# Optimization experiments

Hardware: AMD Instinct MI355X
Metric: run time of the kernel (lower is better)

## Reference

```python
import jax, jax.numpy as jnp
import numpy as np

MARGIN = 70.0
THR = 125.0
PD_EPS = 1e-6  # torch F.pairwise_distance default eps


def _return_cam(features, weight_softmax, class_idx):
    # features: [bz, nc, h, w]; weight_softmax: [n_cls, nc]; class_idx: [bz]
    w_sel = weight_softmax[class_idx]                     # [bz, nc]
    cam = jnp.einsum('bc,bchw->bhw', w_sel, features)     # [bz, h, w]
    cam = cam - cam.min(axis=(1, 2), keepdims=True)
    cam = cam / cam.max(axis=(1, 2), keepdims=True) * 255.0
    return cam[:, None]                                   # [bz, 1, h, w]


def _pairwise_distance(x, y):
    # torch F.pairwise_distance: ||x - y + eps||_2 along last dim
    return jnp.sqrt(jnp.sum((x - y + PD_EPS) ** 2, axis=-1))


def setup_inputs() -> dict:
    key = jax.random.key(0)
    ks = jax.random.split(key, 6)
    bz, nc, h, w, n_cls = 64, 2048, 14, 14, 1000
    return {
        'pred': jax.random.normal(ks[0], (bz, n_cls), jnp.float32),
        'cla_truth': jax.random.randint(ks[1], (bz,), 0, n_cls, jnp.int32),
        'seg_truth': jax.random.uniform(ks[2], (bz, h, w), jnp.float32),
        'features_blobs': jax.random.normal(ks[3], (bz, nc, h, w), jnp.float32),
        'weight_softmax': jax.random.normal(ks[4], (n_cls, nc), jnp.float32),
        'idx': jax.random.randint(ks[5], (bz, 3), 0, n_cls, jnp.int32),
    }


def reference(pred, cla_truth, seg_truth, features_blobs, weight_softmax, idx):
    bz, nc, h, w = features_blobs.shape
    # cross entropy
    logp = jax.nn.log_softmax(pred, axis=-1)
    loss1 = -jnp.mean(logp[jnp.arange(bz), cla_truth])
    # CAMs for top-3 predicted classes
    cam0 = _return_cam(features_blobs, weight_softmax, idx[:, 0])  # [bz,1,h,w]
    cam1 = _return_cam(features_blobs, weight_softmax, idx[:, 1])
    cam2 = _return_cam(features_blobs, weight_softmax, idx[:, 2])
    # binarize cam0 (values in [0,255]); <=thr -> 0, >thr -> 1
    dst = jnp.where(cam0[:, 0] > THR, 1.0, 0.0)                     # [bz,h,w]
    # row-wise distance to seg truth, averaged over rows
    ed1 = jnp.mean(_pairwise_distance(dst, seg_truth), axis=1)      # [bz]
    # CAM-weighted features via broadcasted matmul (requires h == w)
    fea0 = jnp.matmul(cam0, features_blobs)                         # [bz,nc,h,w]
    fea1 = jnp.matmul(cam1, features_blobs)
    fea2 = jnp.matmul(cam2, features_blobs)
    d01 = _pairwise_distance(fea0.reshape(bz, -1), fea1.reshape(bz, -1)) / nc
    d02 = _pairwise_distance(fea0.reshape(bz, -1), fea2.reshape(bz, -1)) / nc
    loss_dis = jnp.mean(ed1 + jnp.clip(MARGIN - d01 - d02, 0.0, None)) + loss1
    return loss_dis
```

## Files before the change

kernel.cpp:

```cpp
#include <hip/hip_runtime.h>
#include <hip/hip_bf16.h>
#include <math.h>

#define BZ      64
#define NC      2048
#define HH      14
#define HW      196
#define NCLS    1000
#define SPLITS  8
#define CPB     (NC/SPLITS)
#define CHUNK   8
#define NCHUNK  (CPB/CHUNK)

#define CAM_OFF  0
#define G_OFF    (BZ*SPLITS*3*HW)
#define S_OFF    (G_OFF + BZ*SPLITS*HW)
#define TERM_OFF (S_OFF + BZ*SPLITS*HH)

__global__ __launch_bounds__(320) void k_stage1(
    const float* __restrict__ F, const float* __restrict__ W,
    const int* __restrict__ idx, float* __restrict__ ws)
{
  __shared__ __align__(16) float Fs[2][CHUNK*HW];
  __shared__ __align__(16) float wls[3][CPB];
  __shared__ __align__(16) float sred[HW];
  __shared__ __align__(16) float gred[224*4];

  const int t = threadIdx.x;
  const int s = blockIdx.x;
  const int b = blockIdx.y;
  const int cbase = s*CPB;

  const int i0 = idx[b*3+0], i1 = idx[b*3+1], i2 = idx[b*3+2];
  if (t < CPB){
    wls[0][t] = W[(size_t)i0*NC + cbase + t];
    wls[1][t] = W[(size_t)i1*NC + cbase + t];
    wls[2][t] = W[(size_t)i2*NC + cbase + t];
  }

  const float* Fb = F + ((size_t)b*NC + cbase)*HW;

  const bool isCam = (t < 49);
  const bool isG   = (t >= 64 && t < 288);
  int m0=0,m1=0,n0=0,n1=0, cg=0, tmKeep=0, tnKeep=0;
  if (isG){
    int g = t - 64;
    int tile = g % 28; cg = g / 28;
    int k = tile, tm = 0;
    while (k >= 7 - tm){ k -= 7 - tm; tm++; }
    int tn = tm + k;
    tmKeep = tm; tnKeep = tn;
    m0 = 2*tm; m1 = m0+1; n0 = 2*tn; n1 = n0+1;
  }
  (void)tmKeep; (void)tnKeep;

  float4 c0a = make_float4(0.f,0.f,0.f,0.f);
  float4 c1a = make_float4(0.f,0.f,0.f,0.f);
  float4 c2a = make_float4(0.f,0.f,0.f,0.f);
  float4 sA  = make_float4(0.f,0.f,0.f,0.f);
  float g00=0.f, g01=0.f, g10=0.f, g11=0.f;

  float4 pre0 = make_float4(0.f,0.f,0.f,0.f);
  float4 pre1 = make_float4(0.f,0.f,0.f,0.f);

  auto loadChunk = [&](int ch){
    if (t < 196){
      const float4* src = (const float4*)(Fb + (size_t)ch*CHUNK*HW);
      pre0 = src[2*t]; pre1 = src[2*t+1];
    }
  };
  auto storeChunk = [&](int bufi){
    if (t < 196){
      float4* dst = (float4*)(&Fs[bufi][0]);
      dst[2*t] = pre0; dst[2*t+1] = pre1;
    }
  };

  loadChunk(0);
  storeChunk(0);
  __syncthreads();

  for (int ch = 0; ch < NCHUNK; ++ch){
    const int bufi = ch & 1;
    if (ch+1 < NCHUNK) loadChunk(ch+1);
    const float* Fsb = &Fs[bufi][0];

    if (isCam){
      float w0a[CHUNK], w1a[CHUNK], w2a[CHUNK];
      *(float4*)&w0a[0] = *(const float4*)&wls[0][ch*CHUNK];
      *(float4*)&w0a[4] = *(const float4*)&wls[0][ch*CHUNK+4];
      *(float4*)&w1a[0] = *(const float4*)&wls[1][ch*CHUNK];
      *(float4*)&w1a[4] = *(const float4*)&wls[1][ch*CHUNK+4];
      *(float4*)&w2a[0] = *(const float4*)&wls[2][ch*CHUNK];
      *(float4*)&w2a[4] = *(const float4*)&wls[2][ch*CHUNK+4];
      #pragma unroll
      for (int c=0;c<CHUNK;c++){
        float4 v = *(const float4*)(Fsb + c*HW + 4*t);
        c0a.x += w0a[c]*v.x; c0a.y += w0a[c]*v.y; c0a.z += w0a[c]*v.z; c0a.w += w0a[c]*v.w;
        c1a.x += w1a[c]*v.x; c1a.y += w1a[c]*v.y; c1a.z += w1a[c]*v.z; c1a.w += w1a[c]*v.w;
        c2a.x += w2a[c]*v.x; c2a.y += w2a[c]*v.y; c2a.z += w2a[c]*v.z; c2a.w += w2a[c]*v.w;
        sA.x += v.x; sA.y += v.y; sA.z += v.z; sA.w += v.w;
      }
    }
    if (isG){
      const float* Mb = Fsb + cg*HW;
      const float2* r0 = (const float2*)(Mb + m0*HH);
      const float2* r1 = (const float2*)(Mb + m1*HH);
      const float2* q0 = (const float2*)(Mb + n0*HH);
      const float2* q1 = (const float2*)(Mb + n1*HH);
      #pragma unroll
      for (int jj=0;jj<7;jj++){
        float2 a0=r0[jj], a1=r1[jj], b0=q0[jj], b1=q1[jj];
        g00 += a0.x*b0.x + a0.y*b0.y;
        g01 += a0.x*b1.x + a0.y*b1.y;
        g10 += a1.x*b0.x + a1.y*b0.y;
        g11 += a1.x*b1.x + a1.y*b1.y;
      }
    }
    if (ch+1 < NCHUNK) storeChunk((ch+1)&1);
    __syncthreads();
  }

  const size_t pslot = (size_t)(b*SPLITS + s);
  if (isCam){
    float* base = ws + CAM_OFF + pslot*3*HW;
    *(float4*)(base          + 4*t) = c0a;
    *(float4*)(base + HW     + 4*t) = c1a;
    *(float4*)(base + 2*HW   + 4*t) = c2a;
    *(float4*)(sred + 4*t) = sA;
  }
  if (isG){
    int g = t - 64;
    float* gr = &gred[g*4];
    gr[0]=g00; gr[1]=g01; gr[2]=g10; gr[3]=g11;
  }
  __syncthreads();

  if (t < HH){
    float acc=0.f;
    #pragma unroll
    for (int j=0;j<HH;j++) acc += sred[t*HH+j];
    ws[S_OFF + pslot*HH + t] = acc;
  }
  if (t < 112){
    int tile = t >> 2, q = t & 3;
    int k = tile, tm2 = 0;
    while (k >= 7 - tm2){ k -= 7 - tm2; tm2++; }
    int tn2 = tm2 + k;
    float acc=0.f;
    #pragma unroll
    for (int c=0;c<8;c++) acc += gred[(c*28+tile)*4 + q];
    int a = q>>1, bb = q&1;
    int mm = 2*tm2 + a, nn = 2*tn2 + bb;
    float* gb = ws + G_OFF + pslot*HW;
    gb[mm*HH+nn] = acc;
    if (tn2 > tm2) gb[nn*HH+mm] = acc;
  }
}

template<int MODE>
__device__ __forceinline__ float bred(float v, float* red){
  #pragma unroll
  for (int o=32;o>0;o>>=1){
    float u = __shfl_down(v, o, 64);
    if (MODE==0) v += u; else if (MODE==1) v = fminf(v,u); else v = fmaxf(v,u);
  }
  __syncthreads();
  if ((threadIdx.x & 63)==0) red[threadIdx.x>>6] = v;
  __syncthreads();
  float r = red[0];
  #pragma unroll
  for (int w=1;w<4;w++){
    float u = red[w];
    if (MODE==0) r += u; else if (MODE==1) r = fminf(r,u); else r = fmaxf(r,u);
  }
  return r;
}

__global__ __launch_bounds__(256) void k_stage2(
    const float* __restrict__ pred, const int* __restrict__ cla,
    const float* __restrict__ seg, float* __restrict__ ws)
{
  const int t = threadIdx.x, b = blockIdx.x;
  __shared__ float cam[3][HW], Gm[HW], Sv[HH];
  __shared__ float D1[HW], D2[HW], EE[HW];
  __shared__ float rowv[HH], dc1[HH], dc2[HH];
  __shared__ float red[4];
  __shared__ float scal[6];

  if (t < HW){
    for (int k=0;k<3;k++){
      float a=0.f;
      for (int s=0;s<SPLITS;s++)
        a += ws[CAM_OFF + ((size_t)(b*SPLITS+s)*3 + k)*HW + t];
      cam[k][t]=a;
    }
    float g=0.f;
    for (int s=0;s<SPLITS;s++) g += ws[G_OFF + (size_t)(b*SPLITS+s)*HW + t];
    Gm[t]=g;
  }
  if (t < HH){
    float a=0.f;
    for (int s=0;s<SPLITS;s++) a += ws[S_OFF + (size_t)(b*SPLITS+s)*HH + t];
    Sv[t]=a;
  }
  __syncthreads();

  for (int k=0;k<3;k++){
    float v = (t<HW)? cam[k][t] : 3.0e38f;
    float mn = bred<1>(v, red);
    v = (t<HW)? cam[k][t] : -3.0e38f;
    float mx = bred<2>(v, red);
    if (t==0){ scal[2*k]=mn; scal[2*k+1]=mx; }
  }
  __syncthreads();

  if (t < HW){
    float c0 = (cam[0][t]-scal[0]) / (scal[1]-scal[0]) * 255.0f;
    float c1 = (cam[1][t]-scal[2]) / (scal[3]-scal[2]) * 255.0f;
    float c2 = (cam[2][t]-scal[4]) / (scal[5]-scal[4]) * 255.0f;
    float dst = (c0 > 125.0f) ? 1.0f : 0.0f;
    D1[t] = c0 - c1; D2[t] = c0 - c2;
    float e = dst - seg[(size_t)b*HW + t] + 1e-6f;
    EE[t] = e*e;
  }
  __syncthreads();

  if (t < HH){
    float rs=0.f, d1=0.f, d2=0.f;
    #pragma unroll
    for (int j=0;j<HH;j++){
      rs += EE[t*HH+j];
      d1 += D1[j*HH+t];
      d2 += D2[j*HH+t];
    }
    rowv[t] = sqrtf(rs); dc1[t]=d1; dc2[t]=d2;
  }
  __syncthreads();

  float v1=0.f, v2=0.f;
  if (t < HW){
    int m = t/HH, mp = t%HH;
    float h1=0.f, h2=0.f;
    #pragma unroll
    for (int i=0;i<HH;i++){
      h1 += D1[i*HH+m]*D1[i*HH+mp];
      h2 += D2[i*HH+m]*D2[i*HH+mp];
    }
    v1 = h1*Gm[t]; v2 = h2*Gm[t];
  }
  float sx2_1 = bred<0>(v1, red);
  float sx2_2 = bred<0>(v2, red);

  const float* pb = pred + (size_t)b*NCLS;
  float mv = -3.0e38f;
  for (int i=t;i<NCLS;i+=256) mv = fmaxf(mv, pb[i]);
  mv = bred<2>(mv, red);
  float es = 0.f;
  for (int i=t;i<NCLS;i+=256) es += expf(pb[i]-mv);
  es = bred<0>(es, red);

  if (t==0){
    float lse = mv + logf(es);
    float ce  = lse - pb[cla[b]];
    float ed1 = 0.f;
    #pragma unroll
    for (int i=0;i<HH;i++) ed1 += rowv[i];
    ed1 *= (1.0f/14.0f);
    float sx1=0.f, sx2=0.f;
    #pragma unroll
    for (int m=0;m<HH;m++){ sx1 += dc1[m]*Sv[m]; sx2 += dc2[m]*Sv[m]; }
    const float NEPS2 = 401408.0f * 1e-12f;
    float d01 = sqrtf(sx2_1 + 2e-6f*sx1 + NEPS2) * (1.0f/2048.0f);
    float d02 = sqrtf(sx2_2 + 2e-6f*sx2 + NEPS2) * (1.0f/2048.0f);
    float term = ed1 + fmaxf(0.0f, 70.0f - d01 - d02) + ce;
    ws[TERM_OFF + b] = term;
  }
}

__global__ void k_stage3(const float* __restrict__ ws, float* __restrict__ out){
  float v = ws[TERM_OFF + threadIdx.x];
  #pragma unroll
  for (int o=32;o>0;o>>=1) v += __shfl_down(v, o, 64);
  if (threadIdx.x==0) out[0] = v * (1.0f/64.0f);
}

extern "C" void kernel_launch(void* const* d_in, const int* in_sizes, int n_in,
                              void* d_out, int out_size, void* d_ws, size_t ws_size,
                              hipStream_t stream) {
  const float* pred = (const float*)d_in[0];
  const int*   cla  = (const int*)  d_in[1];
  const float* seg  = (const float*)d_in[2];
  const float* F    = (const float*)d_in[3];
  const float* W    = (const float*)d_in[4];
  const int*   idx  = (const int*)  d_in[5];
  float* out = (float*)d_out;
  float* ws  = (float*)d_ws;

  dim3 g1(SPLITS, BZ);
  k_stage1<<<g1, 320, 0, stream>>>(F, W, idx, ws);
  k_stage2<<<BZ, 256, 0, stream>>>(pred, cla, seg, ws);
  k_stage3<<<1, 64, 0, stream>>>(ws, out);
}
```

Baseline: 180.1 us.

## Restructure stage1 so each thread owns a column and accumulates full Gram

Rewrites the stage-1 kernel so every thread handles one channel and one column of the 14x14 map. It holds the column in registers and accumulates three CAM rows, the row sum and all 105 symmetric Gram products locally. The chunk size doubles to 16 channels and the block shrinks to 256 threads, with results reduced through shared memory afterwards. The aim is to reuse each feature value across all Gram and CAM outputs and keep all threads busy. The cost is heavy register pressure, possible spills, lower occupancy from the larger shared buffers, and a longer reduction epilogue.

```diff
diff --git a/kernel.cpp b/kernel.cpp
--- a/kernel.cpp
+++ b/kernel.cpp
@@ -9,22 +9,23 @@
 #define NCLS    1000
 #define SPLITS  8
 #define CPB     (NC/SPLITS)
-#define CHUNK   8
-#define NCHUNK  (CPB/CHUNK)
+#define CHN     16
+#define NCHUNK  (CPB/CHN)
+#define NCT     224
 
 #define CAM_OFF  0
 #define G_OFF    (BZ*SPLITS*3*HW)
 #define S_OFF    (G_OFF + BZ*SPLITS*HW)
 #define TERM_OFF (S_OFF + BZ*SPLITS*HH)
 
-__global__ __launch_bounds__(320) void k_stage1(
+__global__ __launch_bounds__(256) void k_stage1(
     const float* __restrict__ F, const float* __restrict__ W,
     const int* __restrict__ idx, float* __restrict__ ws)
 {
-  __shared__ __align__(16) float Fs[2][CHUNK*HW];
+  __shared__ __align__(16) float Fs[2][CHN*HW];
   __shared__ __align__(16) float wls[3][CPB];
-  __shared__ __align__(16) float sred[HW];
-  __shared__ __align__(16) float gred[224*4];
+  __shared__ __align__(16) float SC[35*225];
+  __shared__ float SCB[224];
 
   const int t = threadIdx.x;
   const int s = blockIdx.x;
@@ -32,48 +33,33 @@
   const int cbase = s*CPB;
 
   const int i0 = idx[b*3+0], i1 = idx[b*3+1], i2 = idx[b*3+2];
-  if (t < CPB){
-    wls[0][t] = W[(size_t)i0*NC + cbase + t];
-    wls[1][t] = W[(size_t)i1*NC + cbase + t];
-    wls[2][t] = W[(size_t)i2*NC + cbase + t];
-  }
+  wls[0][t] = W[(size_t)i0*NC + cbase + t];
+  wls[1][t] = W[(size_t)i1*NC + cbase + t];
+  wls[2][t] = W[(size_t)i2*NC + cbase + t];
 
   const float* Fb = F + ((size_t)b*NC + cbase)*HW;
 
-  const bool isCam = (t < 49);
-  const bool isG   = (t >= 64 && t < 288);
-  int m0=0,m1=0,n0=0,n1=0, cg=0, tmKeep=0, tnKeep=0;
-  if (isG){
-    int g = t - 64;
-    int tile = g % 28; cg = g / 28;
-    int k = tile, tm = 0;
-    while (k >= 7 - tm){ k -= 7 - tm; tm++; }
-    int tn = tm + k;
-    tmKeep = tm; tnKeep = tn;
-    m0 = 2*tm; m1 = m0+1; n0 = 2*tn; n1 = n0+1;
-  }
-  (void)tmKeep; (void)tnKeep;
-
-  float4 c0a = make_float4(0.f,0.f,0.f,0.f);
-  float4 c1a = make_float4(0.f,0.f,0.f,0.f);
-  float4 c2a = make_float4(0.f,0.f,0.f,0.f);
-  float4 sA  = make_float4(0.f,0.f,0.f,0.f);
-  float g00=0.f, g01=0.f, g10=0.f, g11=0.f;
-
-  float4 pre0 = make_float4(0.f,0.f,0.f,0.f);
-  float4 pre1 = make_float4(0.f,0.f,0.f,0.f);
-
+  const bool isC = (t < NCT);
+  const int cg = t / 14;
+  const int jj = t % 14;
+
+  float gacc[105];
+  float cam0[14], cam1[14], cam2[14], sacc[14];
+  #pragma unroll
+  for (int e=0;e<105;e++) gacc[e]=0.f;
+  #pragma unroll
+  for (int m=0;m<14;m++){ cam0[m]=0.f; cam1[m]=0.f; cam2[m]=0.f; sacc[m]=0.f; }
+
+  float4 pre0, pre1, pre2, pre3;
   auto loadChunk = [&](int ch){
-    if (t < 196){
-      const float4* src = (const float4*)(Fb + (size_t)ch*CHUNK*HW);
-      pre0 = src[2*t]; pre1 = src[2*t+1];
-    }
+    const float4* src = (const float4*)Fb + (size_t)ch*784;
+    pre0 = src[t]; pre1 = src[t+256]; pre2 = src[t+512];
+    if (t < 16) pre3 = src[t+768];
   };
   auto storeChunk = [&](int bufi){
-    if (t < 196){
-      float4* dst = (float4*)(&Fs[bufi][0]);
-      dst[2*t] = pre0; dst[2*t+1] = pre1;
-    }
+    float4* dst = (float4*)&Fs[bufi][0];
+    dst[t]=pre0; dst[t+256]=pre1; dst[t+512]=pre2;
+    if (t < 16) dst[t+768]=pre3;
   };
 
   loadChunk(0);
@@ -83,78 +69,100 @@
   for (int ch = 0; ch < NCHUNK; ++ch){
     const int bufi = ch & 1;
     if (ch+1 < NCHUNK) loadChunk(ch+1);
-    const float* Fsb = &Fs[bufi][0];
-
-    if (isCam){
-      float w0a[CHUNK], w1a[CHUNK], w2a[CHUNK];
-      *(float4*)&w0a[0] = *(const float4*)&wls[0][ch*CHUNK];
-      *(float4*)&w0a[4] = *(const float4*)&wls[0][ch*CHUNK+4];
-      *(float4*)&w1a[0] = *(const float4*)&wls[1][ch*CHUNK];
-      *(float4*)&w1a[4] = *(const float4*)&wls[1][ch*CHUNK+4];
-      *(float4*)&w2a[0] = *(const float4*)&wls[2][ch*CHUNK];
-      *(float4*)&w2a[4] = *(const float4*)&wls[2][ch*CHUNK+4];
-      #pragma unroll
-      for (int c=0;c<CHUNK;c++){
-        float4 v = *(const float4*)(Fsb + c*HW + 4*t);
-        c0a.x += w0a[c]*v.x; c0a.y += w0a[c]*v.y; c0a.z += w0a[c]*v.z; c0a.w += w0a[c]*v.w;
-        c1a.x += w1a[c]*v.x; c1a.y += w1a[c]*v.y; c1a.z += w1a[c]*v.z; c1a.w += w1a[c]*v.w;
-        c2a.x += w2a[c]*v.x; c2a.y += w2a[c]*v.y; c2a.z += w2a[c]*v.z; c2a.w += w2a[c]*v.w;
-        sA.x += v.x; sA.y += v.y; sA.z += v.z; sA.w += v.w;
+
+    if (isC){
+      const float w0 = wls[0][ch*CHN + cg];
+      const float w1 = wls[1][ch*CHN + cg];
+      const float w2 = wls[2][ch*CHN + cg];
+      const float* base = &Fs[bufi][cg*HW + jj];
+      float v[14];
+      #pragma unroll
+      for (int m=0;m<14;m++) v[m] = base[m*14];
+      #pragma unroll
+      for (int m=0;m<14;m++){
+        sacc[m] += v[m];
+        cam0[m] += w0*v[m];
+        cam1[m] += w1*v[m];
+        cam2[m] += w2*v[m];
       }
-    }
-    if (isG){
-      const float* Mb = Fsb + cg*HW;
-      const float2* r0 = (const float2*)(Mb + m0*HH);
-      const float2* r1 = (const float2*)(Mb + m1*HH);
-      const float2* q0 = (const float2*)(Mb + n0*HH);
-      const float2* q1 = (const float2*)(Mb + n1*HH);
-      #pragma unroll
-      for (int jj=0;jj<7;jj++){
-        float2 a0=r0[jj], a1=r1[jj], b0=q0[jj], b1=q1[jj];
-        g00 += a0.x*b0.x + a0.y*b0.y;
-        g01 += a0.x*b1.x + a0.y*b1.y;
-        g10 += a1.x*b0.x + a1.y*b0.y;
-        g11 += a1.x*b1.x + a1.y*b1.y;
+      int e=0;
+      #pragma unroll
+      for (int m=0;m<14;m++){
+        #pragma unroll
+        for (int mp=m;mp<14;mp++){ gacc[e] += v[m]*v[mp]; e++; }
       }
     }
+
     if (ch+1 < NCHUNK) storeChunk((ch+1)&1);
     __syncthreads();
   }
 
   const size_t pslot = (size_t)(b*SPLITS + s);
-  if (isCam){
-    float* base = ws + CAM_OFF + pslot*3*HW;
-    *(float4*)(base          + 4*t) = c0a;
-    *(float4*)(base + HW     + 4*t) = c1a;
-    *(float4*)(base + 2*HW   + 4*t) = c2a;
-    *(float4*)(sred + 4*t) = sA;
-  }
-  if (isG){
-    int g = t - 64;
-    float* gr = &gred[g*4];
-    gr[0]=g00; gr[1]=g01; gr[2]=g10; gr[3]=g11;
-  }
-  __syncthreads();
-
+
+  #pragma unroll
+  for (int r=0;r<3;r++){
+    if (isC){
+      #pragma unroll
+      for (int el=0; el<35; el++) SC[el*225 + t] = gacc[r*35 + el];
+    }
+    __syncthreads();
+    if (t < 210){
+      const int el = t / 6, g = t % 6;
+      const int start = g*38, len = (g==5)? 34 : 38;
+      float a = 0.f;
+      for (int i=0;i<len;i++) a += SC[el*225 + start + i];
+      SCB[el*6 + g] = a;
+    }
+    __syncthreads();
+    if (t < 35){
+      float a = 0.f;
+      #pragma unroll
+      for (int g=0; g<6; g++) a += SCB[t*6 + g];
+      int e = r*35 + t, m = 0, rem = e;
+      while (rem >= 14 - m){ rem -= 14 - m; m++; }
+      int mp = m + rem;
+      float* gb = ws + G_OFF + pslot*HW;
+      gb[m*HH + mp] = a;
+      if (mp > m) gb[mp*HH + m] = a;
+    }
+    __syncthreads();
+  }
+
+  #pragma unroll
+  for (int k=0;k<3;k++){
+    if (isC){
+      #pragma unroll
+      for (int m=0;m<14;m++)
+        SC[(m*14 + jj)*17 + cg] = (k==0)? cam0[m] : (k==1)? cam1[m] : cam2[m];
+    }
+    __syncthreads();
+    if (t < HW){
+      float a = 0.f;
+      #pragma unroll
+      for (int i=0;i<16;i++) a += SC[t*17 + i];
+      ws[CAM_OFF + pslot*3*HW + k*HW + t] = a;
+    }
+    __syncthreads();
+  }
+
+  if (isC){
+    #pragma unroll
+    for (int m=0;m<14;m++) SC[m*225 + t] = sacc[m];
+  }
+  __syncthreads();
+  if (t < NCT){
+    const int m = t % 14, g = t / 14;
+    float a = 0.f;
+    #pragma unroll
+    for (int i=0;i<14;i++) a += SC[m*225 + g*14 + i];
+    SCB[m*16 + g] = a;
+  }
+  __syncthreads();
   if (t < HH){
-    float acc=0.f;
-    #pragma unroll
-    for (int j=0;j<HH;j++) acc += sred[t*HH+j];
-    ws[S_OFF + pslot*HH + t] = acc;
-  }
-  if (t < 112){
-    int tile = t >> 2, q = t & 3;
-    int k = tile, tm2 = 0;
-    while (k >= 7 - tm2){ k -= 7 - tm2; tm2++; }
-    int tn2 = tm2 + k;
-    float acc=0.f;
-    #pragma unroll
-    for (int c=0;c<8;c++) acc += gred[(c*28+tile)*4 + q];
-    int a = q>>1, bb = q&1;
-    int mm = 2*tm2 + a, nn = 2*tn2 + bb;
-    float* gb = ws + G_OFF + pslot*HW;
-    gb[mm*HH+nn] = acc;
-    if (tn2 > tm2) gb[nn*HH+mm] = acc;
+    float a = 0.f;
+    #pragma unroll
+    for (int g=0; g<16; g++) a += SCB[t*16 + g];
+    ws[S_OFF + pslot*HH + t] = a;
   }
 }
 
@@ -298,7 +306,7 @@
   float* ws  = (float*)d_ws;
 
   dim3 g1(SPLITS, BZ);
-  k_stage1<<<g1, 320, 0, stream>>>(F, W, idx, ws);
+  k_stage1<<<g1, 256, 0, stream>>>(F, W, idx, ws);
   k_stage2<<<BZ, 256, 0, stream>>>(pred, cla, seg, ws);
   k_stage3<<<1, 64, 0, stream>>>(ws, out);
 }
```

Measured after the change: 183.3 us. No clear change (+1.8%).
